# Kernel optimization log

Hardware: AMD Instinct MI355X
Metric: run time of the kernel (lower is better)

The kernel has to match this reference:

```python
import jax, jax.numpy as jnp
import numpy as np

N_NODES = 50000
N_EDGES = 800000
IN_CH, HID_CH, OUT_CH = 128, 256, 128


def setup_inputs() -> dict:
    key = jax.random.key(0)
    ks = jax.random.split(key, 9)
    x = jax.random.normal(ks[0], (N_NODES, IN_CH), dtype=jnp.float32)
    edge_index = jax.random.randint(ks[1], (2, N_EDGES), 0, N_NODES, dtype=jnp.int64)
    # SAGEConv params: lin_l (aggregated neighbors, with bias), lin_r (root, no bias)
    s1 = 1.0 / np.sqrt(IN_CH)
    s2 = 1.0 / np.sqrt(HID_CH)
    W1_l = jax.random.uniform(ks[2], (IN_CH, HID_CH), jnp.float32, -s1, s1)
    W1_r = jax.random.uniform(ks[3], (IN_CH, HID_CH), jnp.float32, -s1, s1)
    b1 = jax.random.uniform(ks[4], (HID_CH,), jnp.float32, -s1, s1)
    W2_l = jax.random.uniform(ks[5], (HID_CH, OUT_CH), jnp.float32, -s2, s2)
    W2_r = jax.random.uniform(ks[6], (HID_CH, OUT_CH), jnp.float32, -s2, s2)
    b2 = jax.random.uniform(ks[7], (OUT_CH,), jnp.float32, -s2, s2)
    return {"x": x, "edge_index": edge_index, "W1_l": W1_l, "W1_r": W1_r,
            "b1": b1, "W2_l": W2_l, "W2_r": W2_r, "b2": b2}


def _sage_conv(x, edge_index, Wl, Wr, b):
    # PyG SAGEConv: out = lin_l(mean_{j in N(i)} x_j) + lin_r(x_i)
    src, dst = edge_index[0], edge_index[1]
    msg = x[src]                                                    # [E, C] gather
    agg = jax.ops.segment_sum(msg, dst, num_segments=x.shape[0])    # [N, C] scatter-add
    cnt = jax.ops.segment_sum(jnp.ones((src.shape[0],), x.dtype), dst,
                              num_segments=x.shape[0])              # [N]
    agg = agg / jnp.maximum(cnt, 1.0)[:, None]                      # mean; deg-0 -> 0
    return agg @ Wl + x @ Wr + b


def reference(x, edge_index, W1_l, W1_r, b1, W2_l, W2_r, b2):
    h = jax.nn.relu(_sage_conv(x, edge_index, W1_l, W1_r, b1))
    # dropout(p=0.5) is stochastic; use eval-mode identity for a deterministic baseline
    out = _sage_conv(h, edge_index, W2_l, W2_r, b2)
    return jax.nn.log_softmax(out, axis=1)
```

## Files before the change

### kernel.cpp

```cpp
#include <hip/hip_runtime.h>
#include <math.h>

#define NN 50000
#define NE 800000
#define BINW 512
#define NB ((NN + BINW - 1) / BINW)
#define CAP 12288
#define CHUNK 4096
#define EPT 16

typedef __attribute__((ext_vector_type(8))) short short8;
typedef __attribute__((ext_vector_type(4))) float f32x4;
typedef unsigned int uint32;

__device__ inline unsigned short f2bf(float f) {
    unsigned u = __builtin_bit_cast(unsigned, f);
    u += 0x7FFF + ((u >> 16) & 1);
    return (unsigned short)(u >> 16);
}
__device__ inline float bf_lo(uint32 v) { return __builtin_bit_cast(float, v << 16); }
__device__ inline float bf_hi(uint32 v) { return __builtin_bit_cast(float, v & 0xFFFF0000u); }

__device__ inline int edge_at(const void* edges, int is64, int i) {
    return is64 ? (int)((const long long*)edges)[i] : ((const int*)edges)[i];
}

__global__ void k_prep(const float* __restrict__ x, unsigned short* __restrict__ A1,
                       const float* __restrict__ W1l, const float* __restrict__ W1r,
                       const float* __restrict__ W2l, const float* __restrict__ W2r,
                       unsigned short* __restrict__ B1t, unsigned short* __restrict__ B2t,
                       int* flag, int* bcnt, const void* edges) {
    int b = blockIdx.x;
    if (b < 6250) {
        int t = b * 256 + threadIdx.x;
        if (t >= NN * 32) return;
        int node = t >> 5, q = t & 31;
        float4 v = *(const float4*)(x + (size_t)node * 128 + q * 4);
        uint32 p0 = f2bf(v.x) | ((uint32)f2bf(v.y) << 16);
        uint32 p1 = f2bf(v.z) | ((uint32)f2bf(v.w) << 16);
        *(uint2*)(A1 + (size_t)node * 256 + 128 + q * 4) = make_uint2(p0, p1);
    } else if (b < 6506) {
        int t = (b - 6250) * 256 + threadIdx.x;
        int n = t >> 8, k = t & 255;
        float v1 = (k < 128) ? W1l[k * 256 + n] : W1r[(k - 128) * 256 + n];
        B1t[n * 256 + k] = f2bf(v1);
        float v2 = (n < 128) ? W2l[k * 128 + n] : W2r[k * 128 + (n - 128)];
        B2t[n * 256 + k] = f2bf(v2);
    } else {
        if (threadIdx.x < NB) bcnt[threadIdx.x] = 0;
        if (threadIdx.x < 64) {
            const long long* q = (const long long*)edges;
            long long v = q[threadIdx.x];
            int ok = (v >= 0 && v < NN) ? 1 : 0;
            unsigned long long m = __ballot(ok);
            if (threadIdx.x == 0) *flag = (m == ~0ull) ? 1 : 0;
        }
    }
}

__global__ __launch_bounds__(256) void k_bin(const void* __restrict__ edges,
                                             const int* __restrict__ flag,
                                             uint32* __restrict__ gbuf,
                                             int* __restrict__ bcnt) {
    __shared__ int hist[NB], excl[NB + 1], cur[NB], gpos[NB];
    __shared__ uint32 sorted[CHUNK];
    int t = threadIdx.x;
    int base = blockIdx.x * CHUNK;
    int n = NE - base; if (n > CHUNK) n = CHUNK;
    int is64 = *flag;
    int sA[EPT], dA[EPT];
    #pragma unroll
    for (int q = 0; q < EPT; ++q) {
        int i = t + q * 256;
        if (i < n) {
            sA[q] = edge_at(edges, is64, base + i);
            dA[q] = edge_at(edges, is64, NE + base + i);
        } else dA[q] = -1;
    }
    for (int i = t; i < NB; i += 256) hist[i] = 0;
    __syncthreads();
    #pragma unroll
    for (int q = 0; q < EPT; ++q)
        if (dA[q] >= 0) atomicAdd(&hist[dA[q] >> 9], 1);
    __syncthreads();
    if (t == 0) {
        int s = 0;
        for (int b = 0; b < NB; ++b) { excl[b] = s; s += hist[b]; }
        excl[NB] = s;
    }
    __syncthreads();
    if (t < NB) {
        gpos[t] = atomicAdd(&bcnt[t], hist[t]);
        cur[t] = excl[t];
    }
    __syncthreads();
    #pragma unroll
    for (int q = 0; q < EPT; ++q) {
        if (dA[q] >= 0) {
            int b = dA[q] >> 9;
            int lp = atomicAdd(&cur[b], 1);
            sorted[lp] = ((uint32)(dA[q] & (BINW - 1)) << 16) | (uint32)sA[q];
        }
    }
    __syncthreads();
    for (int i = t; i < n; i += 256) {
        int lo = 0, hi = NB - 1;
        while (lo < hi) { int mid = (lo + hi + 1) >> 1; if (excl[mid] <= i) lo = mid; else hi = mid - 1; }
        int gp = gpos[lo] + (i - excl[lo]);
        if (gp < CAP) gbuf[(size_t)lo * CAP + gp] = sorted[i];
    }
}

__global__ void k_bbase(const int* __restrict__ bcnt, int* __restrict__ bbase,
                        int* __restrict__ offs) {
    if (threadIdx.x == 0) {
        int s = 0;
        for (int b = 0; b < NB; ++b) { bbase[b] = s; s += bcnt[b]; }
        offs[NN] = s;
    }
}

__global__ __launch_bounds__(256) void k_sort(const uint32* __restrict__ gbuf,
                                              const int* __restrict__ bcnt,
                                              const int* __restrict__ bbase,
                                              int* __restrict__ offs,
                                              unsigned short* __restrict__ ssrc) {
    __shared__ int hist[BINW], cur[BINW], wsum[4];
    __shared__ int sorted[CAP];
    int b = blockIdx.x, t = threadIdx.x;
    int cnt = bcnt[b]; if (cnt > CAP) cnt = CAP;
    int nbase = b * BINW;
    int ncnt = NN - nbase; if (ncnt > BINW) ncnt = BINW;
    for (int i = t; i < BINW; i += 256) hist[i] = 0;
    __syncthreads();
    for (int i = t; i < cnt; i += 256)
        atomicAdd(&hist[gbuf[(size_t)b * CAP + i] >> 16], 1);
    __syncthreads();
    int lane = t & 63, w = t >> 6;
    int d0 = hist[2 * t], d1 = hist[2 * t + 1];
    int v = d0 + d1;
    #pragma unroll
    for (int d = 1; d < 64; d <<= 1) { int x = __shfl_up(v, d); if (lane >= d) v += x; }
    if (lane == 63) wsum[w] = v;
    __syncthreads();
    if (t == 0) { int s = 0; for (int i = 0; i < 4; ++i) { int x = wsum[i]; wsum[i] = s; s += x; } }
    __syncthreads();
    int e0 = wsum[w] + (v - d0 - d1);
    int e1 = e0 + d0;
    if (2 * t < ncnt)     offs[nbase + 2 * t]     = bbase[b] + e0;
    if (2 * t + 1 < ncnt) offs[nbase + 2 * t + 1] = bbase[b] + e1;
    cur[2 * t] = e0; cur[2 * t + 1] = e1;
    __syncthreads();
    for (int i = t; i < cnt; i += 256) {
        uint32 p = gbuf[(size_t)b * CAP + i];
        int lp = atomicAdd(&cur[p >> 16], 1);
        sorted[lp] = (int)(p & 0xFFFFu);
    }
    __syncthreads();
    for (int i = t; i < cnt; i += 256)
        ssrc[bbase[b] + i] = (unsigned short)sorted[i];
}

#define ACC8(vv) { a[0] += bf_lo((vv).x); a[1] += bf_hi((vv).x); \
                   a[2] += bf_lo((vv).y); a[3] += bf_hi((vv).y); \
                   a[4] += bf_lo((vv).z); a[5] += bf_hi((vv).z); \
                   a[6] += bf_lo((vv).w); a[7] += bf_hi((vv).w); }

__device__ inline void burst_gather4(const unsigned short* __restrict__ tab, int coff,
                                     const unsigned short* __restrict__ ssrc, int s0, int s1,
                                     int lane, float* a) {
    int grp = lane >> 4, cl = lane & 15;
    const unsigned short* bp = tab + coff + cl * 8;
    int e = s0;
    while (e < s1) {
        int cnt = s1 - e; if (cnt > 64) cnt = 64;
        int myidx = (lane < cnt) ? (int)ssrc[e + lane] : 0;
        for (int r0 = 0; r0 < cnt; r0 += 16) {
            uint4 v[4]; bool ok[4];
            #pragma unroll
            for (int u = 0; u < 4; ++u) {
                int r = r0 + u * 4 + grp;
                ok[u] = r < cnt;
                int s = __shfl(myidx, r & 63);
                v[u] = *(const uint4*)(bp + (size_t)s * 256);
            }
            #pragma unroll
            for (int u = 0; u < 4; ++u) if (ok[u]) ACC8(v[u]);
        }
        e += cnt;
    }
}

__device__ inline void xreduce8(float* a) {
    #pragma unroll
    for (int k = 0; k < 8; ++k) {
        a[k] += __shfl_xor(a[k], 16);
        a[k] += __shfl_xor(a[k], 32);
    }
}

__global__ void k_agg(unsigned short* __restrict__ A1, const int* __restrict__ offs,
                      const unsigned short* __restrict__ ssrc) {
    int node = blockIdx.x * 4 + (threadIdx.x >> 6);
    int lane = threadIdx.x & 63;
    if (node >= NN) return;
    int cl = lane & 15;
    int s0 = offs[node], s1 = offs[node + 1];
    float a[8] = {};
    burst_gather4(A1, 128, ssrc, s0, s1, lane, a);
    xreduce8(a);
    float inv = 1.0f / fmaxf((float)(s1 - s0), 1.0f);
    if (lane < 16) {
        uint4 p;
        p.x = f2bf(a[0] * inv) | ((uint32)f2bf(a[1] * inv) << 16);
        p.y = f2bf(a[2] * inv) | ((uint32)f2bf(a[3] * inv) << 16);
        p.z = f2bf(a[4] * inv) | ((uint32)f2bf(a[5] * inv) << 16);
        p.w = f2bf(a[6] * inv) | ((uint32)f2bf(a[7] * inv) << 16);
        *(uint4*)(A1 + (size_t)node * 256 + cl * 8) = p;
    }
}

template <bool RELU>
__global__ __launch_bounds__(256)
void k_gemm_bf(const unsigned short* __restrict__ A, const unsigned short* __restrict__ Bt,
               const float* __restrict__ bias, unsigned short* __restrict__ C) {
    constexpr int LDK = 40;
    __shared__ unsigned short Asm[2][128][LDK];
    __shared__ unsigned short Bsm[2][128][LDK];
    int t = threadIdx.x;
    int lane = t & 63, w = t >> 6;
    int m0 = blockIdx.x * 128, n0 = blockIdx.y * 128;
    int wr = (w >> 1) * 64, wc = (w & 1) * 64;
    int fr = lane & 15, fk = (lane >> 4) * 8;

    f32x4 acc[4][4] = {};
    int ml = t >> 2, sub = t & 3;
    int gmA0 = m0 + ml, gmA1 = m0 + ml + 64;
    bool okA0 = gmA0 < NN, okA1 = gmA1 < NN;
    const short8* pa0 = (const short8*)(A + (size_t)gmA0 * 256 + sub * 8);
    const short8* pa1 = (const short8*)(A + (size_t)gmA1 * 256 + sub * 8);
    const short8* pb0 = (const short8*)(Bt + (size_t)(n0 + ml) * 256 + sub * 8);
    const short8* pb1 = (const short8*)(Bt + (size_t)(n0 + ml + 64) * 256 + sub * 8);
    const short8 zero = {};

    short8 va0, va1, vb0, vb1;
    auto LOAD = [&](int ks) {
        va0 = okA0 ? pa0[ks * 4] : zero;
        va1 = okA1 ? pa1[ks * 4] : zero;
        vb0 = pb0[ks * 4];
        vb1 = pb1[ks * 4];
    };
    auto STORE = [&](int buf) {
        *(short8*)&Asm[buf][ml][sub * 8]      = va0;
        *(short8*)&Asm[buf][ml + 64][sub * 8] = va1;
        *(short8*)&Bsm[buf][ml][sub * 8]      = vb0;
        *(short8*)&Bsm[buf][ml + 64][sub * 8] = vb1;
    };

    LOAD(0);
    STORE(0);
    __syncthreads();
    int cur = 0;
    #pragma unroll
    for (int ks = 0; ks < 8; ++ks) {
        if (ks < 7) LOAD(ks + 1);
        short8 af[4], bfr[4];
        #pragma unroll
        for (int i = 0; i < 4; ++i) af[i] = *(const short8*)&Asm[cur][wr + i * 16 + fr][fk];
        #pragma unroll
        for (int j = 0; j < 4; ++j) bfr[j] = *(const short8*)&Bsm[cur][wc + j * 16 + fr][fk];
        #pragma unroll
        for (int i = 0; i < 4; ++i)
            #pragma unroll
            for (int j = 0; j < 4; ++j)
                acc[i][j] = __builtin_amdgcn_mfma_f32_16x16x32_bf16(af[i], bfr[j], acc[i][j], 0, 0, 0);
        if (ks < 7) {
            STORE(cur ^ 1);
            __syncthreads();
            cur ^= 1;
        }
    }

    int r0 = (lane >> 4) * 4;
    #pragma unroll
    for (int i = 0; i < 4; ++i) {
        #pragma unroll
        for (int j = 0; j < 4; ++j) {
            int gn = n0 + wc + j * 16 + fr;
            float bb = RELU ? bias[gn] : 0.f;
            #pragma unroll
            for (int rr = 0; rr < 4; ++rr) {
                int gm = m0 + wr + i * 16 + r0 + rr;
                if (gm >= NN) continue;
                float v = acc[i][j][rr];
                if (RELU) v = fmaxf(v + bb, 0.f);
                C[(size_t)gm * 256 + gn] = f2bf(v);
            }
        }
    }
}

__global__ void k_final(const unsigned short* __restrict__ P, const int* __restrict__ offs,
                        const unsigned short* __restrict__ ssrc, const float* __restrict__ b2,
                        float* __restrict__ out) {
    int node = blockIdx.x * 4 + (threadIdx.x >> 6);
    int lane = threadIdx.x & 63;
    if (node >= NN) return;
    int cl = lane & 15;
    int s0 = offs[node], s1 = offs[node + 1];
    float a[8] = {};
    burst_gather4(P, 0, ssrc, s0, s1, lane, a);
    xreduce8(a);
    float inv = 1.0f / fmaxf((float)(s1 - s0), 1.0f);
    uint4 rv = *(const uint4*)(P + (size_t)node * 256 + 128 + cl * 8);
    float4 ba = *(const float4*)(b2 + cl * 8);
    float4 bb = *(const float4*)(b2 + cl * 8 + 4);
    float vv[8];
    vv[0] = a[0] * inv + bf_lo(rv.x) + ba.x;
    vv[1] = a[1] * inv + bf_hi(rv.x) + ba.y;
    vv[2] = a[2] * inv + bf_lo(rv.y) + ba.z;
    vv[3] = a[3] * inv + bf_hi(rv.y) + ba.w;
    vv[4] = a[4] * inv + bf_lo(rv.z) + bb.x;
    vv[5] = a[5] * inv + bf_hi(rv.z) + bb.y;
    vv[6] = a[6] * inv + bf_lo(rv.w) + bb.z;
    vv[7] = a[7] * inv + bf_hi(rv.w) + bb.w;

    float mx = vv[0];
    #pragma unroll
    for (int k = 1; k < 8; ++k) mx = fmaxf(mx, vv[k]);
    #pragma unroll
    for (int d = 1; d < 16; d <<= 1) mx = fmaxf(mx, __shfl_xor(mx, d));
    float s = 0.f;
    #pragma unroll
    for (int k = 0; k < 8; ++k) s += __expf(vv[k] - mx);
    #pragma unroll
    for (int d = 1; d < 16; d <<= 1) s += __shfl_xor(s, d);
    float ls = logf(s);
    if (lane < 16) {
        float4 o0 = make_float4(vv[0] - mx - ls, vv[1] - mx - ls, vv[2] - mx - ls, vv[3] - mx - ls);
        float4 o1 = make_float4(vv[4] - mx - ls, vv[5] - mx - ls, vv[6] - mx - ls, vv[7] - mx - ls);
        *(float4*)(out + (size_t)node * 128 + cl * 8) = o0;
        *(float4*)(out + (size_t)node * 128 + cl * 8 + 4) = o1;
    }
}

extern "C" void kernel_launch(void* const* d_in, const int* in_sizes, int n_in,
                              void* d_out, int out_size, void* d_ws, size_t ws_size,
                              hipStream_t stream) {
    const float* x   = (const float*)d_in[0];
    const void*  edg = d_in[1];
    const float* W1l = (const float*)d_in[2];
    const float* W1r = (const float*)d_in[3];
    const float* b1  = (const float*)d_in[4];
    const float* W2l = (const float*)d_in[5];
    const float* W2r = (const float*)d_in[6];
    const float* b2  = (const float*)d_in[7];
    float* out = (float*)d_out;

    char* ws = (char*)d_ws;
    size_t off = 0;
    auto alloc = [&](size_t bytes) {
        size_t cur = off;
        off = (off + bytes + 255) & ~(size_t)255;
        return cur;
    };
    int* flag  = (int*)(ws + alloc(4));
    int* bcnt  = (int*)(ws + alloc((size_t)NB * 4));
    int* bbase = (int*)(ws + alloc((size_t)NB * 4));
    int* offs  = (int*)(ws + alloc((size_t)(NN + 1) * 4));
    unsigned short* ssrc = (unsigned short*)(ws + alloc((size_t)NE * 2));
    uint32* gbuf = (uint32*)(ws + alloc((size_t)NB * CAP * 4));
    unsigned short* A1  = (unsigned short*)(ws + alloc((size_t)NN * 256 * 2));
    unsigned short* Hb  = (unsigned short*)(ws + alloc((size_t)NN * 256 * 2));
    unsigned short* Pb  = (unsigned short*)(ws + alloc((size_t)NN * 256 * 2));
    unsigned short* B1t = (unsigned short*)(ws + alloc((size_t)65536 * 2));
    unsigned short* B2t = (unsigned short*)(ws + alloc((size_t)65536 * 2));

    int nb_w = (NN + 3) / 4;
    int mblocks = (NN + 127) / 128;
    int binblocks = (NE + CHUNK - 1) / CHUNK;

    k_prep<<<6507, 256, 0, stream>>>(x, A1, W1l, W1r, W2l, W2r, B1t, B2t, flag, bcnt, edg);
    k_bin<<<binblocks, 256, 0, stream>>>(edg, flag, gbuf, bcnt);
    k_bbase<<<1, 64, 0, stream>>>(bcnt, bbase, offs);
    k_sort<<<NB, 256, 0, stream>>>(gbuf, bcnt, bbase, offs, ssrc);
    k_agg<<<nb_w, 256, 0, stream>>>(A1, offs, ssrc);
    k_gemm_bf<true><<<dim3(mblocks, 2), 256, 0, stream>>>(A1, B1t, b1, Hb);
    k_gemm_bf<false><<<dim3(mblocks, 2), 256, 0, stream>>>(Hb, B2t, nullptr, Pb);
    k_final<<<nb_w, 256, 0, stream>>>(Pb, offs, ssrc, b2, out);
}
```

Baseline: 157.2 us.

## Fuse prep with edge binning, drop global atomics, use direct-to-LDS GEMM loads

Merges the input conversion, weight transpose and edge binning into one front kernel and replaces global atomic bin reservation plus a serial base kernel with a per-chunk count matrix that the sort kernel prefix-sums itself. The sort kernel scatters directly to the output instead of through an LDS staging pass. The GEMM stages tiles with global_load_lds instead of register round-trips, and the neighbor gather unrolls deeper. Risks include unpadded LDS layout causing bank conflicts and unguarded reads past the last row relying on workspace padding.

```diff
diff --git a/kernel.cpp b/kernel.cpp
--- a/kernel.cpp
+++ b/kernel.cpp
@@ -5,13 +5,18 @@
 #define NE 800000
 #define BINW 512
 #define NB ((NN + BINW - 1) / BINW)
-#define CAP 12288
+#define CAP 10240
 #define CHUNK 4096
+#define NBIN ((NE + CHUNK - 1) / CHUNK)
+#define NXB 6250
+#define NWB 256
 #define EPT 16
 
 typedef __attribute__((ext_vector_type(8))) short short8;
 typedef __attribute__((ext_vector_type(4))) float f32x4;
 typedef unsigned int uint32;
+typedef __attribute__((address_space(3))) unsigned int lds_uint;
+typedef const __attribute__((address_space(1))) unsigned int glb_uint;
 
 __device__ inline unsigned short f2bf(float f) {
     unsigned u = __builtin_bit_cast(unsigned, f);
@@ -25,49 +30,47 @@
     return is64 ? (int)((const long long*)edges)[i] : ((const int*)edges)[i];
 }
 
-__global__ void k_prep(const float* __restrict__ x, unsigned short* __restrict__ A1,
-                       const float* __restrict__ W1l, const float* __restrict__ W1r,
-                       const float* __restrict__ W2l, const float* __restrict__ W2r,
-                       unsigned short* __restrict__ B1t, unsigned short* __restrict__ B2t,
-                       int* flag, int* bcnt, const void* edges) {
+__global__ __launch_bounds__(256)
+void k_front(const void* __restrict__ edges, uint32* __restrict__ gbuf,
+             int* __restrict__ cnt,
+             const float* __restrict__ x, unsigned short* __restrict__ A1,
+             const float* __restrict__ W1l, const float* __restrict__ W1r,
+             const float* __restrict__ W2l, const float* __restrict__ W2r,
+             unsigned short* __restrict__ B1t, unsigned short* __restrict__ B2t) {
     int b = blockIdx.x;
-    if (b < 6250) {
-        int t = b * 256 + threadIdx.x;
-        if (t >= NN * 32) return;
-        int node = t >> 5, q = t & 31;
-        float4 v = *(const float4*)(x + (size_t)node * 128 + q * 4);
-        uint32 p0 = f2bf(v.x) | ((uint32)f2bf(v.y) << 16);
-        uint32 p1 = f2bf(v.z) | ((uint32)f2bf(v.w) << 16);
-        *(uint2*)(A1 + (size_t)node * 256 + 128 + q * 4) = make_uint2(p0, p1);
-    } else if (b < 6506) {
-        int t = (b - 6250) * 256 + threadIdx.x;
-        int n = t >> 8, k = t & 255;
-        float v1 = (k < 128) ? W1l[k * 256 + n] : W1r[(k - 128) * 256 + n];
-        B1t[n * 256 + k] = f2bf(v1);
-        float v2 = (n < 128) ? W2l[k * 128 + n] : W2r[k * 128 + (n - 128)];
-        B2t[n * 256 + k] = f2bf(v2);
-    } else {
-        if (threadIdx.x < NB) bcnt[threadIdx.x] = 0;
-        if (threadIdx.x < 64) {
-            const long long* q = (const long long*)edges;
-            long long v = q[threadIdx.x];
-            int ok = (v >= 0 && v < NN) ? 1 : 0;
-            unsigned long long m = __ballot(ok);
-            if (threadIdx.x == 0) *flag = (m == ~0ull) ? 1 : 0;
-        }
-    }
-}
-
-__global__ __launch_bounds__(256) void k_bin(const void* __restrict__ edges,
-                                             const int* __restrict__ flag,
-                                             uint32* __restrict__ gbuf,
-                                             int* __restrict__ bcnt) {
-    __shared__ int hist[NB], excl[NB + 1], cur[NB], gpos[NB];
+    if (b >= NBIN) {
+        if (b < NBIN + NXB) {
+            int t = (b - NBIN) * 256 + threadIdx.x;
+            if (t >= NN * 32) return;
+            int node = t >> 5, q = t & 31;
+            float4 v = *(const float4*)(x + (size_t)node * 128 + q * 4);
+            uint32 p0 = f2bf(v.x) | ((uint32)f2bf(v.y) << 16);
+            uint32 p1 = f2bf(v.z) | ((uint32)f2bf(v.w) << 16);
+            *(uint2*)(A1 + (size_t)node * 256 + 128 + q * 4) = make_uint2(p0, p1);
+        } else {
+            int t = (b - NBIN - NXB) * 256 + threadIdx.x;
+            int n = t >> 8, k = t & 255;
+            float v1 = (k < 128) ? W1l[k * 256 + n] : W1r[(k - 128) * 256 + n];
+            B1t[n * 256 + k] = f2bf(v1);
+            float v2 = (n < 128) ? W2l[k * 128 + n] : W2r[k * 128 + (n - 128)];
+            B2t[n * 256 + k] = f2bf(v2);
+        }
+        return;
+    }
+    __shared__ int hist[NB], excl[NB], cur[NB], is64s;
     __shared__ uint32 sorted[CHUNK];
     int t = threadIdx.x;
-    int base = blockIdx.x * CHUNK;
+    int base = b * CHUNK;
     int n = NE - base; if (n > CHUNK) n = CHUNK;
-    int is64 = *flag;
+    if (t < 64) {
+        const long long* q = (const long long*)edges;
+        long long v = q[t];
+        unsigned long long m = __ballot(v >= 0 && v < NN);
+        if (t == 0) is64s = (m == ~0ull) ? 1 : 0;
+    }
+    for (int i = t; i < NB; i += 256) hist[i] = 0;
+    __syncthreads();
+    int is64 = is64s;
     int sA[EPT], dA[EPT];
     #pragma unroll
     for (int q = 0; q < EPT; ++q) {
@@ -77,64 +80,72 @@
             dA[q] = edge_at(edges, is64, NE + base + i);
         } else dA[q] = -1;
     }
-    for (int i = t; i < NB; i += 256) hist[i] = 0;
-    __syncthreads();
     #pragma unroll
     for (int q = 0; q < EPT; ++q)
         if (dA[q] >= 0) atomicAdd(&hist[dA[q] >> 9], 1);
     __syncthreads();
     if (t == 0) {
         int s = 0;
-        for (int b = 0; b < NB; ++b) { excl[b] = s; s += hist[b]; }
-        excl[NB] = s;
+        for (int k = 0; k < NB; ++k) { excl[k] = s; s += hist[k]; }
     }
     __syncthreads();
     if (t < NB) {
-        gpos[t] = atomicAdd(&bcnt[t], hist[t]);
         cur[t] = excl[t];
+        cnt[b * NB + t] = hist[t];
     }
     __syncthreads();
     #pragma unroll
     for (int q = 0; q < EPT; ++q) {
         if (dA[q] >= 0) {
-            int b = dA[q] >> 9;
-            int lp = atomicAdd(&cur[b], 1);
-            sorted[lp] = ((uint32)(dA[q] & (BINW - 1)) << 16) | (uint32)sA[q];
-        }
-    }
-    __syncthreads();
-    for (int i = t; i < n; i += 256) {
-        int lo = 0, hi = NB - 1;
-        while (lo < hi) { int mid = (lo + hi + 1) >> 1; if (excl[mid] <= i) lo = mid; else hi = mid - 1; }
-        int gp = gpos[lo] + (i - excl[lo]);
-        if (gp < CAP) gbuf[(size_t)lo * CAP + gp] = sorted[i];
-    }
-}
-
-__global__ void k_bbase(const int* __restrict__ bcnt, int* __restrict__ bbase,
-                        int* __restrict__ offs) {
-    if (threadIdx.x == 0) {
-        int s = 0;
-        for (int b = 0; b < NB; ++b) { bbase[b] = s; s += bcnt[b]; }
-        offs[NN] = s;
-    }
+            int bk = dA[q] >> 9;
+            int lp = atomicAdd(&cur[bk], 1);
+            sorted[lp] = ((uint32)bk << 25) | ((uint32)(dA[q] & (BINW - 1)) << 16) | (uint32)sA[q];
+        }
+    }
+    __syncthreads();
+    for (int i = t; i < n; i += 256) gbuf[(size_t)base + i] = sorted[i];
 }
 
 __global__ __launch_bounds__(256) void k_sort(const uint32* __restrict__ gbuf,
-                                              const int* __restrict__ bcnt,
-                                              const int* __restrict__ bbase,
+                                              const int* __restrict__ cnt,
                                               int* __restrict__ offs,
                                               unsigned short* __restrict__ ssrc) {
     __shared__ int hist[BINW], cur[BINW], wsum[4];
-    __shared__ int sorted[CAP];
+    __shared__ int startr[NBIN], segbase[NBIN + 1];
+    __shared__ int seq[CAP];
+    __shared__ int bbase_s;
     int b = blockIdx.x, t = threadIdx.x;
-    int cnt = bcnt[b]; if (cnt > CAP) cnt = CAP;
     int nbase = b * BINW;
     int ncnt = NN - nbase; if (ncnt > BINW) ncnt = BINW;
+    if (t < NBIN) {
+        int s = 0;
+        const int* row = cnt + t * NB;
+        for (int k = 0; k < b; ++k) s += row[k];
+        startr[t] = s;
+    }
     for (int i = t; i < BINW; i += 256) hist[i] = 0;
     __syncthreads();
-    for (int i = t; i < cnt; i += 256)
-        atomicAdd(&hist[gbuf[(size_t)b * CAP + i] >> 16], 1);
+    if (t == 0) {
+        int s = 0, bb = 0;
+        for (int blk = 0; blk < NBIN; ++blk) {
+            bb += startr[blk];
+            segbase[blk] = s;
+            s += cnt[blk * NB + b];
+        }
+        segbase[NBIN] = s;
+        bbase_s = bb;
+    }
+    __syncthreads();
+    int cnt_b = segbase[NBIN]; if (cnt_b > CAP) cnt_b = CAP;
+    int bbase = bbase_s;
+    for (int pos = t; pos < cnt_b; pos += 256) {
+        int lo = 0, hi = NBIN - 1;
+        while (lo < hi) { int mid = (lo + hi + 1) >> 1; if (segbase[mid] <= pos) lo = mid; else hi = mid - 1; }
+        uint32 v = gbuf[(size_t)lo * CHUNK + startr[lo] + (pos - segbase[lo])];
+        v &= 0x1FFFFFFu;
+        seq[pos] = (int)v;
+        atomicAdd(&hist[v >> 16], 1);
+    }
     __syncthreads();
     int lane = t & 63, w = t >> 6;
     int d0 = hist[2 * t], d1 = hist[2 * t + 1];
@@ -147,18 +158,16 @@
     __syncthreads();
     int e0 = wsum[w] + (v - d0 - d1);
     int e1 = e0 + d0;
-    if (2 * t < ncnt)     offs[nbase + 2 * t]     = bbase[b] + e0;
-    if (2 * t + 1 < ncnt) offs[nbase + 2 * t + 1] = bbase[b] + e1;
+    if (2 * t < ncnt)     offs[nbase + 2 * t]     = bbase + e0;
+    if (2 * t + 1 < ncnt) offs[nbase + 2 * t + 1] = bbase + e1;
     cur[2 * t] = e0; cur[2 * t + 1] = e1;
-    __syncthreads();
-    for (int i = t; i < cnt; i += 256) {
-        uint32 p = gbuf[(size_t)b * CAP + i];
+    if (b == NB - 1 && t == 0) offs[NN] = bbase + cnt_b;
+    __syncthreads();
+    for (int pos = t; pos < cnt_b; pos += 256) {
+        int p = seq[pos];
         int lp = atomicAdd(&cur[p >> 16], 1);
-        sorted[lp] = (int)(p & 0xFFFFu);
-    }
-    __syncthreads();
-    for (int i = t; i < cnt; i += 256)
-        ssrc[bbase[b] + i] = (unsigned short)sorted[i];
+        ssrc[bbase + lp] = (unsigned short)(p & 0xFFFF);
+    }
 }
 
 #define ACC8(vv) { a[0] += bf_lo((vv).x); a[1] += bf_hi((vv).x); \
@@ -175,17 +184,17 @@
     while (e < s1) {
         int cnt = s1 - e; if (cnt > 64) cnt = 64;
         int myidx = (lane < cnt) ? (int)ssrc[e + lane] : 0;
-        for (int r0 = 0; r0 < cnt; r0 += 16) {
-            uint4 v[4]; bool ok[4];
+        for (int r0 = 0; r0 < cnt; r0 += 32) {
+            uint4 v[8]; bool ok[8];
             #pragma unroll
-            for (int u = 0; u < 4; ++u) {
+            for (int u = 0; u < 8; ++u) {
                 int r = r0 + u * 4 + grp;
                 ok[u] = r < cnt;
                 int s = __shfl(myidx, r & 63);
                 v[u] = *(const uint4*)(bp + (size_t)s * 256);
             }
             #pragma unroll
-            for (int u = 0; u < 4; ++u) if (ok[u]) ACC8(v[u]);
+            for (int u = 0; u < 8; ++u) if (ok[u]) ACC8(v[u]);
         }
         e += cnt;
     }
@@ -224,9 +233,8 @@
 __global__ __launch_bounds__(256)
 void k_gemm_bf(const unsigned short* __restrict__ A, const unsigned short* __restrict__ Bt,
                const float* __restrict__ bias, unsigned short* __restrict__ C) {
-    constexpr int LDK = 40;
-    __shared__ unsigned short Asm[2][128][LDK];
-    __shared__ unsigned short Bsm[2][128][LDK];
+    __shared__ unsigned short AsmL[2][128 * 32];
+    __shared__ unsigned short BsmL[2][128 * 32];
     int t = threadIdx.x;
     int lane = t & 63, w = t >> 6;
     int m0 = blockIdx.x * 128, n0 = blockIdx.y * 128;
@@ -234,48 +242,37 @@
     int fr = lane & 15, fk = (lane >> 4) * 8;
 
     f32x4 acc[4][4] = {};
-    int ml = t >> 2, sub = t & 3;
-    int gmA0 = m0 + ml, gmA1 = m0 + ml + 64;
-    bool okA0 = gmA0 < NN, okA1 = gmA1 < NN;
-    const short8* pa0 = (const short8*)(A + (size_t)gmA0 * 256 + sub * 8);
-    const short8* pa1 = (const short8*)(A + (size_t)gmA1 * 256 + sub * 8);
-    const short8* pb0 = (const short8*)(Bt + (size_t)(n0 + ml) * 256 + sub * 8);
-    const short8* pb1 = (const short8*)(Bt + (size_t)(n0 + ml + 64) * 256 + sub * 8);
-    const short8 zero = {};
-
-    short8 va0, va1, vb0, vb1;
-    auto LOAD = [&](int ks) {
-        va0 = okA0 ? pa0[ks * 4] : zero;
-        va1 = okA1 ? pa1[ks * 4] : zero;
-        vb0 = pb0[ks * 4];
-        vb1 = pb1[ks * 4];
+    int srow = lane >> 2;
+    int scol = (lane & 3) * 8;
+    auto STAGE = [&](int bufi, int ks) {
+        #pragma unroll
+        for (int q = 0; q < 2; ++q) {
+            int widx = w * 2 + q;
+            int row = widx * 16 + srow;
+            const unsigned short* ga = A + (size_t)(m0 + row) * 256 + ks * 32 + scol;
+            __builtin_amdgcn_global_load_lds((glb_uint*)ga, (lds_uint*)&AsmL[bufi][widx * 512], 16, 0, 0);
+            const unsigned short* gb = Bt + (size_t)(n0 + row) * 256 + ks * 32 + scol;
+            __builtin_amdgcn_global_load_lds((glb_uint*)gb, (lds_uint*)&BsmL[bufi][widx * 512], 16, 0, 0);
+        }
     };
-    auto STORE = [&](int buf) {
-        *(short8*)&Asm[buf][ml][sub * 8]      = va0;
-        *(short8*)&Asm[buf][ml + 64][sub * 8] = va1;
-        *(short8*)&Bsm[buf][ml][sub * 8]      = vb0;
-        *(short8*)&Bsm[buf][ml + 64][sub * 8] = vb1;
-    };
-
-    LOAD(0);
-    STORE(0);
+
+    STAGE(0, 0);
     __syncthreads();
     int cur = 0;
     #pragma unroll
     for (int ks = 0; ks < 8; ++ks) {
-        if (ks < 7) LOAD(ks + 1);
+        if (ks < 7) STAGE(cur ^ 1, ks + 1);
         short8 af[4], bfr[4];
         #pragma unroll
-        for (int i = 0; i < 4; ++i) af[i] = *(const short8*)&Asm[cur][wr + i * 16 + fr][fk];
-        #pragma unroll
-        for (int j = 0; j < 4; ++j) bfr[j] = *(const short8*)&Bsm[cur][wc + j * 16 + fr][fk];
+        for (int i = 0; i < 4; ++i) af[i] = *(const short8*)&AsmL[cur][(wr + i * 16 + fr) * 32 + fk];
+        #pragma unroll
+        for (int j = 0; j < 4; ++j) bfr[j] = *(const short8*)&BsmL[cur][(wc + j * 16 + fr) * 32 + fk];
         #pragma unroll
         for (int i = 0; i < 4; ++i)
             #pragma unroll
             for (int j = 0; j < 4; ++j)
                 acc[i][j] = __builtin_amdgcn_mfma_f32_16x16x32_bf16(af[i], bfr[j], acc[i][j], 0, 0, 0);
         if (ks < 7) {
-            STORE(cur ^ 1);
             __syncthreads();
             cur ^= 1;
         }
@@ -364,26 +361,23 @@
         off = (off + bytes + 255) & ~(size_t)255;
         return cur;
     };
-    int* flag  = (int*)(ws + alloc(4));
-    int* bcnt  = (int*)(ws + alloc((size_t)NB * 4));
-    int* bbase = (int*)(ws + alloc((size_t)NB * 4));
+    int* cnt   = (int*)(ws + alloc((size_t)NBIN * NB * 4));
     int* offs  = (int*)(ws + alloc((size_t)(NN + 1) * 4));
     unsigned short* ssrc = (unsigned short*)(ws + alloc((size_t)NE * 2));
-    uint32* gbuf = (uint32*)(ws + alloc((size_t)NB * CAP * 4));
+    uint32* gbuf = (uint32*)(ws + alloc((size_t)NBIN * CHUNK * 4));
     unsigned short* A1  = (unsigned short*)(ws + alloc((size_t)NN * 256 * 2));
     unsigned short* Hb  = (unsigned short*)(ws + alloc((size_t)NN * 256 * 2));
     unsigned short* Pb  = (unsigned short*)(ws + alloc((size_t)NN * 256 * 2));
     unsigned short* B1t = (unsigned short*)(ws + alloc((size_t)65536 * 2));
     unsigned short* B2t = (unsigned short*)(ws + alloc((size_t)65536 * 2));
+    (void)alloc(65536);
 
     int nb_w = (NN + 3) / 4;
     int mblocks = (NN + 127) / 128;
-    int binblocks = (NE + CHUNK - 1) / CHUNK;
-
-    k_prep<<<6507, 256, 0, stream>>>(x, A1, W1l, W1r, W2l, W2r, B1t, B2t, flag, bcnt, edg);
-    k_bin<<<binblocks, 256, 0, stream>>>(edg, flag, gbuf, bcnt);
-    k_bbase<<<1, 64, 0, stream>>>(bcnt, bbase, offs);
-    k_sort<<<NB, 256, 0, stream>>>(gbuf, bcnt, bbase, offs, ssrc);
+
+    k_front<<<NBIN + NXB + NWB, 256, 0, stream>>>(edg, gbuf, cnt, x, A1,
+                                                  W1l, W1r, W2l, W2r, B1t, B2t);
+    k_sort<<<NB, 256, 0, stream>>>(gbuf, cnt, offs, ssrc);
     k_agg<<<nb_w, 256, 0, stream>>>(A1, offs, ssrc);
     k_gemm_bf<true><<<dim3(mblocks, 2), 256, 0, stream>>>(A1, B1t, b1, Hb);
     k_gemm_bf<false><<<dim3(mblocks, 2), 256, 0, stream>>>(Hb, B2t, nullptr, Pb);
```

New measurement: 179.8 us. 1.14x slower.
